# Kernel tuning notes

Measured on AMD Instinct MI355X. Metric: run time of the kernel, lower is better.

The kernel has to match this reference:

```python
import jax, jax.numpy as jnp
from jax import lax
import numpy as np

V = 30000   # vocab_size
E = 64      # embedding_dim
H = 64      # lstm_units
K = 9       # num_tags
B = 512
T = 512


def setup_inputs() -> dict:
    key = jax.random.key(0)
    ks = jax.random.split(key, 12)
    s = 0.05
    return {
        "tokens": jax.random.randint(ks[0], (B, T), 0, V),
        "emb":   jax.random.normal(ks[1], (V + 1, E), dtype=jnp.float32) * s,
        "Wf": jax.random.normal(ks[2], (E, 4 * H), dtype=jnp.float32) * s,
        "Uf": jax.random.normal(ks[3], (H, 4 * H), dtype=jnp.float32) * s,
        "bf": jnp.zeros((4 * H,), dtype=jnp.float32),
        "Wb": jax.random.normal(ks[4], (E, 4 * H), dtype=jnp.float32) * s,
        "Ub": jax.random.normal(ks[5], (H, 4 * H), dtype=jnp.float32) * s,
        "bb": jnp.zeros((4 * H,), dtype=jnp.float32),
        "Wd": jax.random.normal(ks[6], (2 * H, K), dtype=jnp.float32) * s,
        "bd": jnp.zeros((K,), dtype=jnp.float32),
        "trans": jax.random.normal(ks[7], (K, K), dtype=jnp.float32) * s,
    }


def _lstm(x_tm, mask_tm, W, U, b):
    """Keras-convention LSTM over time-major x_tm [T,B,E]; masked steps carry state."""
    Bsz = x_tm.shape[1]
    h0 = jnp.zeros((Bsz, U.shape[0]), x_tm.dtype)
    c0 = jnp.zeros_like(h0)

    def step(carry, inp):
        h, c = carry
        xt, mt = inp                      # xt [B,E], mt [B] bool
        z = xt @ W + h @ U + b            # [B,4H], gate order i,f,g,o
        i, f, g, o = jnp.split(z, 4, axis=-1)
        c_new = jax.nn.sigmoid(f) * c + jax.nn.sigmoid(i) * jnp.tanh(g)
        h_new = jax.nn.sigmoid(o) * jnp.tanh(c_new)
        m = mt[:, None]
        h2 = jnp.where(m, h_new, h)
        c2 = jnp.where(m, c_new, c)
        return (h2, c2), h2

    _, hs = lax.scan(step, (h0, c0), (x_tm, mask_tm))
    return hs                              # [T,B,H]


def _viterbi(pot, mask, trans):
    """Batched Viterbi decode. pot [B,T,K], mask [B,T] bool, trans [K,K]."""
    pot_t = pot.transpose(1, 0, 2)         # [T,B,K]
    m_t = mask.T                           # [T,B]
    alpha0 = pot_t[0]
    ident = jnp.arange(K, dtype=jnp.int32)[None, :]

    def step(alpha, inp):
        p, m = inp                         # p [B,K], m [B]
        scores = alpha[:, :, None] + trans[None]   # [B, prev K, next K]
        best = scores.max(axis=1)
        bp = scores.argmax(axis=1).astype(jnp.int32)
        mm = m[:, None]
        alpha_new = jnp.where(mm, best + p, alpha)
        bp = jnp.where(mm, bp, ident)
        return alpha_new, bp

    alpha, bps = lax.scan(step, alpha0, (pot_t[1:], m_t[1:]))   # bps [T-1,B,K]
    last = alpha.argmax(axis=-1).astype(jnp.int32)              # [B]

    def back(tag, bp):
        prev = jnp.take_along_axis(bp, tag[:, None], axis=1)[:, 0]
        return prev, prev

    _, ys = lax.scan(back, last, bps, reverse=True)             # ys[t] = tag_t, t<T-1
    tags = jnp.concatenate([ys, last[None]], axis=0).T          # [B,T]
    return jnp.where(mask, tags, 0)


def reference(tokens, emb, Wf, Uf, bf, Wb, Ub, bb, Wd, bd, trans):
    mask = tokens != 0                     # mask_zero semantics
    x = emb[tokens]                        # [B,T,E]
    x_tm = x.transpose(1, 0, 2)            # [T,B,E]
    m_tm = mask.T
    hf = _lstm(x_tm, m_tm, Wf, Uf, bf)                     # forward dir
    hb = _lstm(x_tm[::-1], m_tm[::-1], Wb, Ub, bb)[::-1]   # backward dir
    h = jnp.concatenate([hf, hb], axis=-1).transpose(1, 0, 2)  # [B,T,2H]
    potentials = h @ Wd + bd               # CRF emission potentials [B,T,K]
    decoded = _viterbi(potentials, mask, trans)
    seq_len = mask.sum(axis=1).astype(jnp.int32)
    return decoded, potentials, seq_len
```

## Files before the change

kernel.cpp:

```cpp
#include <hip/hip_runtime.h>

#define BB 512
#define TT 512
#define KK 9
#define VP1 30001
#define BTK ((size_t)BB * TT * KK)

typedef __attribute__((ext_vector_type(8))) short short8;
typedef __attribute__((ext_vector_type(4))) float float4v;

__device__ __forceinline__ float sigm(float x) {
    return __builtin_amdgcn_rcpf(1.0f + __expf(-x));
}
__device__ __forceinline__ float tanh_(float x) {
    return 1.0f - 2.0f * __builtin_amdgcn_rcpf(__expf(2.0f * x) + 1.0f);
}

__device__ __forceinline__ unsigned short f2bf(float f) {
    unsigned int u = __float_as_uint(f);
    unsigned int r = u + 0x7fffu + ((u >> 16) & 1u);
    return (unsigned short)(r >> 16);
}
__device__ __forceinline__ float bflo2f(unsigned int d) { return __uint_as_float(d << 16); }
__device__ __forceinline__ float bfhi2f(unsigned int d) { return __uint_as_float(d & 0xffff0000u); }

__device__ __forceinline__ float bcast(float v, int i) {
    return __uint_as_float(__builtin_amdgcn_readlane(__float_as_uint(v), i));
}

__device__ __forceinline__ void block_sync_lds() {
    __builtin_amdgcn_s_waitcnt(0xC07F);
    __builtin_amdgcn_s_barrier();
}

__global__ __launch_bounds__(256)
void wswz_kernel(const float* __restrict__ Wf, const float* __restrict__ bfv,
                 const float* __restrict__ Wb, const float* __restrict__ bbv,
                 unsigned short* __restrict__ wswz, float* __restrict__ bsw)
{
    const int tid = threadIdx.x;
#pragma unroll
    for (int it = 0; it < 16; ++it) {
        int o = blockIdx.x * 4096 + it * 256 + tid;
        int k = o & 63, c = o >> 6;
        int dir = c >> 8, rem = c & 255;
        int u = rem >> 2, g = rem & 3;
        float val = (dir ? Wb : Wf)[k * 256 + g * 64 + u];
        wswz[o] = f2bf(val);
    }
    if (blockIdx.x == 0) {
#pragma unroll
        for (int h = 0; h < 2; ++h) {
            int c = h * 256 + tid;
            int dir = c >> 8, rem = c & 255;
            bsw[c] = (dir ? bbv : bfv)[(rem & 3) * 64 + (rem >> 2)];
        }
    }
}

__global__ __launch_bounds__(256, 1)
void embw_kernel(const float* __restrict__ emb,
                 const unsigned short* __restrict__ wswz, const float* __restrict__ bsw,
                 unsigned short* __restrict__ embw)
{
    const int v0 = blockIdx.x * 64;
    const int tid = threadIdx.x;
    const int w = tid >> 6, lane = tid & 63;
    const int l16 = lane & 15, quad = lane >> 4;

    __shared__ __align__(16) unsigned short clds[64][520];

    short8 bFr[8][2];
    float biasn[8];
#pragma unroll
    for (int n = 0; n < 8; ++n) {
        int c = w * 128 + n * 16 + l16;
        biasn[n] = bsw[c];
        const unsigned short* wp = wswz + c * 64;
#pragma unroll
        for (int q = 0; q < 2; ++q)
            bFr[n][q] = *(const short8*)(wp + q * 32 + quad * 8);
    }

    short8 aFr[4][2];
#pragma unroll
    for (int mt = 0; mt < 4; ++mt) {
        int vrow = v0 + mt * 16 + l16;
        if (vrow >= VP1) vrow = VP1 - 1;
        const float* er = emb + (size_t)vrow * 64;
#pragma unroll
        for (int q = 0; q < 2; ++q) {
            const float* p = er + q * 32 + quad * 8;
            float4 x0 = *(const float4*)(p);
            float4 x1 = *(const float4*)(p + 4);
            short8 v;
            v[0] = (short)f2bf(x0.x); v[1] = (short)f2bf(x0.y);
            v[2] = (short)f2bf(x0.z); v[3] = (short)f2bf(x0.w);
            v[4] = (short)f2bf(x1.x); v[5] = (short)f2bf(x1.y);
            v[6] = (short)f2bf(x1.z); v[7] = (short)f2bf(x1.w);
            aFr[mt][q] = v;
        }
    }

    float4v acc[4][8];
#pragma unroll
    for (int mt = 0; mt < 4; ++mt)
#pragma unroll
        for (int n = 0; n < 8; ++n) {
            acc[mt][n][0] = biasn[n]; acc[mt][n][1] = biasn[n];
            acc[mt][n][2] = biasn[n]; acc[mt][n][3] = biasn[n];
        }
#pragma unroll
    for (int mt = 0; mt < 4; ++mt)
#pragma unroll
        for (int n = 0; n < 8; ++n) {
            acc[mt][n] = __builtin_amdgcn_mfma_f32_16x16x32_bf16(aFr[mt][0], bFr[n][0], acc[mt][n], 0, 0, 0);
            acc[mt][n] = __builtin_amdgcn_mfma_f32_16x16x32_bf16(aFr[mt][1], bFr[n][1], acc[mt][n], 0, 0, 0);
        }

#pragma unroll
    for (int mt = 0; mt < 4; ++mt)
#pragma unroll
        for (int n = 0; n < 8; ++n) {
            int cc = w * 128 + n * 16 + l16;
#pragma unroll
            for (int r = 0; r < 4; ++r)
                clds[mt * 16 + quad * 4 + r][cc] = f2bf(acc[mt][n][r]);
        }
    __syncthreads();

#pragma unroll
    for (int it = 0; it < 16; ++it) {
        int idx = it * 256 + tid;
        int row = idx >> 6, chunk = idx & 63;
        if (v0 + row < VP1) {
            uint4 val = *(const uint4*)&clds[row][chunk * 8];
            *(uint4*)(embw + (size_t)(v0 + row) * 512 + chunk * 8) = val;
        }
    }
}

__global__ __launch_bounds__(256, 1)
void rec_kernel(const int* __restrict__ tokens,
                const unsigned short* __restrict__ embw,
                const float* __restrict__ Uf, const float* __restrict__ Ub,
                const float* __restrict__ Wd,
                float* __restrict__ potf, float* __restrict__ potb)
{
    const int blk = blockIdx.x;
    const int dir = blk >> 7;
    const int row0 = (blk & 127) * 4;
    const int tid = threadIdx.x;
    const int lane = tid & 63;
    const int w = tid >> 6;
    const int l16 = lane & 15, quad = lane >> 4;
    const int u = w * 16 + l16;

    const float* Up = dir ? Ub : Uf;
    float* pot = dir ? potb : potf;
    const uint2* ebase = (const uint2*)embw + dir * 64 + u;

    __shared__ int tokl[4][TT];
    __shared__ __align__(16) unsigned short hl[2][16][72];

    for (int i = tid; i < 2 * 16 * 72; i += 256)
        ((unsigned short*)hl)[i] = 0;
    for (int i = tid; i < 4 * TT; i += 256) {
        int r = i >> 9, t = i & 511;
        tokl[r][t] = tokens[(row0 + r) * TT + t];
    }

    short8 bU[4][2];
#pragma unroll
    for (int g = 0; g < 4; ++g)
#pragma unroll
        for (int q = 0; q < 2; ++q) {
            short8 v;
#pragma unroll
            for (int j = 0; j < 8; ++j) {
                int k = q * 32 + quad * 8 + j;
                v[j] = (short)f2bf(Up[k * 256 + g * 64 + u]);
            }
            bU[g][q] = v;
        }
    short8 bW[2];
#pragma unroll
    for (int q = 0; q < 2; ++q) {
        short8 v;
#pragma unroll
        for (int j = 0; j < 8; ++j) {
            int k = q * 32 + quad * 8 + j;
            v[j] = (l16 < KK) ? (short)f2bf(Wd[(dir * 64 + k) * KK + l16]) : (short)0;
        }
        bW[q] = v;
    }

    __syncthreads();

    int tokA[4], tokB[4];
    uint2 zxp[4];
#pragma unroll
    for (int d = 0; d < 4; ++d) {
        int td = dir ? (TT - 1 - d) : d;
        int td4 = dir ? (TT - 1 - (d + 4)) : (d + 4);
        tokA[d] = tokl[quad][td];
        tokB[d] = tokl[quad][td4];
    }
#pragma unroll
    for (int d = 0; d < 4; ++d)
        zxp[d] = ebase[(size_t)tokA[d] << 7];

    float c_st = 0.f, h_st = 0.f;

    float4v accg[4];
#pragma unroll
    for (int g = 0; g < 4; ++g) {
        accg[g][0] = 0.f; accg[g][1] = 0.f; accg[g][2] = 0.f; accg[g][3] = 0.f;
    }

    const int tprev0 = dir ? (w == 0 ? TT - 4 : TT - w) : (w == 0 ? 3 : w - 1);
    int vOff = (((row0 + quad) * TT + tprev0) * KK + l16) * 4;
    const int vStep = (dir ? -4 : 4) * KK * 4;

    for (int sb = 0; sb < TT; sb += 4) {
#pragma unroll
        for (int ss = 0; ss < 4; ++ss) {
            const int s = sb + ss;
            int tcur = tokA[ss];
            uint2 zcur = zxp[ss];

            hl[ss & 1][quad * 4][u] = f2bf(h_st);

            if (s + 4 < TT)
                zxp[ss] = ebase[(size_t)tokB[ss] << 7];
            tokA[ss] = tokB[ss];

            block_sync_lds();

            const unsigned short* hrow = &hl[ss & 1][l16][0];
            short8 a0 = *(const short8*)(hrow + quad * 8);
            short8 a1 = *(const short8*)(hrow + 32 + quad * 8);

            if (s + 8 < TT) {
                int t8 = dir ? (TT - 1 - (s + 8)) : (s + 8);
                tokB[ss] = tokl[quad][t8];
            }

            accg[0][0] = bflo2f(zcur.x);
            accg[1][0] = bfhi2f(zcur.x);
            accg[2][0] = bflo2f(zcur.y);
            accg[3][0] = bfhi2f(zcur.y);
#pragma unroll
            for (int g = 0; g < 4; ++g) {
                accg[g] = __builtin_amdgcn_mfma_f32_16x16x32_bf16(a0, bU[g][0], accg[g], 0, 0, 0);
                accg[g] = __builtin_amdgcn_mfma_f32_16x16x32_bf16(a1, bU[g][1], accg[g], 0, 0, 0);
            }

            if (w == ss && s > 0) {
                float4v accP = {0.f, 0.f, 0.f, 0.f};
                accP = __builtin_amdgcn_mfma_f32_16x16x32_bf16(a0, bW[0], accP, 0, 0, 0);
                accP = __builtin_amdgcn_mfma_f32_16x16x32_bf16(a1, bW[1], accP, 0, 0, 0);
                if (l16 < KK)
                    *(float*)((char*)pot + vOff) = accP[0];
                vOff += vStep;
            }

            {
                float zi = accg[0][0], zf = accg[1][0], zg = accg[2][0], zo = accg[3][0];
                float cn = sigm(zf) * c_st + sigm(zi) * tanh_(zg);
                float hn = sigm(zo) * tanh_(cn);
                bool m = (tcur != 0);
                h_st = m ? hn : h_st;
                c_st = m ? cn : c_st;
            }
        }
    }

    hl[0][quad * 4][u] = f2bf(h_st);
    block_sync_lds();
    if (w == 0) {
        const unsigned short* hrow = &hl[0][l16][0];
        short8 a0 = *(const short8*)(hrow + quad * 8);
        short8 a1 = *(const short8*)(hrow + 32 + quad * 8);
        float4v accP = {0.f, 0.f, 0.f, 0.f};
        accP = __builtin_amdgcn_mfma_f32_16x16x32_bf16(a0, bW[0], accP, 0, 0, 0);
        accP = __builtin_amdgcn_mfma_f32_16x16x32_bf16(a1, bW[1], accP, 0, 0, 0);
        int tlast = dir ? 0 : (TT - 1);
        if (l16 < KK)
            pot[((size_t)(row0 + quad) * TT + tlast) * KK + l16] = accP[0];
    }
}

__global__ __launch_bounds__(64)
void viterbi_kernel(const int* __restrict__ tokens,
                    const float* __restrict__ potf, const float* __restrict__ potb,
                    const float* __restrict__ bd, const float* __restrict__ trans,
                    float* __restrict__ dec_out, float* __restrict__ pot_out,
                    float* __restrict__ seq_out)
{
    const int row = blockIdx.x;
    const int lane = threadIdx.x;

    __shared__ float pl[TT * KK + 16];
    __shared__ unsigned char bpl[(TT - 1) * KK];
    __shared__ unsigned char maskl[TT + 8];
    __shared__ unsigned char segmap[64][KK];
    __shared__ unsigned char bseq[65];
    __shared__ float decl_[TT];
    __shared__ float bdl[16];

    if (lane < KK) bdl[lane] = bd[lane];
    if (lane < 8) maskl[TT + lane] = 0;
    pl[TT * KK + lane % 16] = 0.f;

    int cnt = 0;
#pragma unroll
    for (int ch = 0; ch < TT / 64; ++ch) {
        int tk = tokens[row * TT + ch * 64 + lane];
        int m = (tk != 0) ? 1 : 0;
        maskl[ch * 64 + lane] = (unsigned char)m;
        cnt += m;
    }
    for (int off = 32; off > 0; off >>= 1) cnt += __shfl_down(cnt, off);
    if (lane == 0) seq_out[row] = (float)cnt;

    const size_t base = (size_t)row * (TT * KK);
    int r9 = lane % KK;
    for (int i = 0; i < (TT * KK) / 64; ++i) {
        int li = i * 64 + lane;
        float s = potf[base + li] + potb[base + li] + bdl[r9];
        pl[li] = s;
        pot_out[base + li] = s;
        r9 = (r9 + 1 == KK) ? 0 : r9 + 1;
    }
    __syncthreads();

    float treg[KK];
#pragma unroll
    for (int i = 0; i < KK; ++i) treg[i] = (lane < KK) ? trans[i * KK + lane] : 0.f;

    float alpha = (lane < KK) ? pl[lane] : -1e30f;
    float pnext = (lane < KK) ? pl[KK + lane] : 0.f;
    int mnext = maskl[1];
#pragma unroll 4
    for (int t = 1; t < TT; ++t) {
        float p = pnext;
        int m = mnext;
        pnext = (lane < KK) ? pl[(t + 1) * KK + lane] : 0.f;
        mnext = maskl[t + 1];

        float sc[KK];
#pragma unroll
        for (int i = 0; i < KK; ++i) sc[i] = bcast(alpha, i) + treg[i];
        float b0 = fmaxf(fmaxf(fmaxf(sc[0], sc[1]), sc[2]),
                   fmaxf(fmaxf(fmaxf(sc[3], sc[4]), sc[5]),
                         fmaxf(fmaxf(sc[6], sc[7]), sc[8])));
        int i0 = 8;
#pragma unroll
        for (int i = 7; i >= 0; --i) i0 = (sc[i] == b0) ? i : i0;

        alpha = m ? (b0 + p) : alpha;
        int bpv = m ? i0 : lane;
        if (lane < KK) bpl[(t - 1) * KK + lane] = (unsigned char)bpv;
    }
    float sc[KK];
#pragma unroll
    for (int i = 0; i < KK; ++i) sc[i] = bcast(alpha, i);
    float b0 = fmaxf(fmaxf(fmaxf(sc[0], sc[1]), sc[2]),
               fmaxf(fmaxf(fmaxf(sc[3], sc[4]), sc[5]),
                     fmaxf(fmaxf(sc[6], sc[7]), sc[8])));
    int last = 8;
#pragma unroll
    for (int i = 7; i >= 0; --i) last = (sc[i] == b0) ? i : last;
    __syncthreads();

    {
        int l = lane;
#pragma unroll
        for (int x = 0; x < KK; ++x) {
            int y = x;
#pragma unroll
            for (int d = 7; d >= 0; --d) {
                int t = 8 * l + d;
                if (t < TT - 1) y = bpl[t * KK + y];
            }
            segmap[l][x] = (unsigned char)y;
        }
    }
    __syncthreads();
    if (lane == 0) {
        int cur = last;
        bseq[64] = (unsigned char)last;
        for (int l = 63; l >= 0; --l) {
            cur = segmap[l][cur];
            bseq[l] = (unsigned char)cur;
        }
    }
    __syncthreads();
    {
        int l = lane;
        int cur = bseq[l + 1];
#pragma unroll
        for (int d = 7; d >= 0; --d) {
            int t = 8 * l + d;
            if (t < TT - 1) cur = bpl[t * KK + cur];
            decl_[t] = (maskl[t] != 0) ? (float)cur : 0.f;
        }
    }
    __syncthreads();
#pragma unroll
    for (int ch = 0; ch < TT / 64; ++ch)
        dec_out[(size_t)row * TT + ch * 64 + lane] = decl_[ch * 64 + lane];
}

extern "C" void kernel_launch(void* const* d_in, const int* in_sizes, int n_in,
                              void* d_out, int out_size, void* d_ws, size_t ws_size,
                              hipStream_t stream)
{
    const int*   tokens = (const int*)d_in[0];
    const float* emb    = (const float*)d_in[1];
    const float* Wf     = (const float*)d_in[2];
    const float* Uf     = (const float*)d_in[3];
    const float* bfv    = (const float*)d_in[4];
    const float* Wb     = (const float*)d_in[5];
    const float* Ub     = (const float*)d_in[6];
    const float* bbv    = (const float*)d_in[7];
    const float* Wd     = (const float*)d_in[8];
    const float* bd     = (const float*)d_in[9];
    const float* trans  = (const float*)d_in[10];

    float* out     = (float*)d_out;
    float* dec_out = out;
    float* pot_out = out + (size_t)BB * TT;
    float* seq_out = out + (size_t)BB * TT + BTK;

    float* potf = (float*)d_ws;
    float* potb = potf + BTK;
    unsigned short* embw = (unsigned short*)(potb + BTK);
    unsigned short* wswz = (unsigned short*)potf;
    float* bsw = (float*)((char*)potf + 512 * 64 * sizeof(unsigned short));

    hipLaunchKernelGGL(wswz_kernel, dim3(8), dim3(256), 0, stream,
                       Wf, bfv, Wb, bbv, wswz, bsw);
    hipLaunchKernelGGL(embw_kernel, dim3(469), dim3(256), 0, stream,
                       emb, wswz, bsw, embw);
    hipLaunchKernelGGL(rec_kernel, dim3(256), dim3(256), 0, stream,
                       tokens, embw, Uf, Ub, Wd, potf, potb);
    hipLaunchKernelGGL(viterbi_kernel, dim3(BB), dim3(64), 0, stream,
                       tokens, potf, potb, bd, trans, dec_out, pot_out, seq_out);
}
```

Before: 401.1 us.

## Run each LSTM recurrence in a single wavefront with bpermute h exchange

The recurrence kernel moves from four wavefronts per block, which shared h through LDS with a block barrier every timestep, to a single 64-lane wavefront that computes all 16 gate column tiles itself. The hidden state is redistributed into the MFMA A-operand layout with ds_bpermute, and the precomputed input projections are re-swizzled to match. This removes per-step barriers and LDS round trips from the serial critical path. In exchange each wave issues four times as many MFMAs per step, holds more registers, and the grid drops to 256 single-wave blocks, so latency per step could rise.

Measured after the change: 727.4 us. +81.3%, slower.

```diff
diff --git a/kernel.cpp b/kernel.cpp
--- a/kernel.cpp
+++ b/kernel.cpp
@@ -8,6 +8,7 @@
 
 typedef __attribute__((ext_vector_type(8))) short short8;
 typedef __attribute__((ext_vector_type(4))) float float4v;
+typedef __attribute__((ext_vector_type(4))) int int4v;
 
 __device__ __forceinline__ float sigm(float x) {
     return __builtin_amdgcn_rcpf(1.0f + __expf(-x));
@@ -26,11 +27,6 @@
 
 __device__ __forceinline__ float bcast(float v, int i) {
     return __uint_as_float(__builtin_amdgcn_readlane(__float_as_uint(v), i));
-}
-
-__device__ __forceinline__ void block_sync_lds() {
-    __builtin_amdgcn_s_waitcnt(0xC07F);
-    __builtin_amdgcn_s_barrier();
 }
 
 __global__ __launch_bounds__(256)
@@ -44,7 +40,9 @@
         int o = blockIdx.x * 4096 + it * 256 + tid;
         int k = o & 63, c = o >> 6;
         int dir = c >> 8, rem = c & 255;
-        int u = rem >> 2, g = rem & 3;
+        int l16p = rem >> 4, idx = rem & 15;
+        int un = idx >> 2, g = idx & 3;
+        int u = un * 16 + l16p;
         float val = (dir ? Wb : Wf)[k * 256 + g * 64 + u];
         wswz[o] = f2bf(val);
     }
@@ -53,7 +51,9 @@
         for (int h = 0; h < 2; ++h) {
             int c = h * 256 + tid;
             int dir = c >> 8, rem = c & 255;
-            bsw[c] = (dir ? bbv : bfv)[(rem & 3) * 64 + (rem >> 2)];
+            int l16p = rem >> 4, idx = rem & 15;
+            int un = idx >> 2, g = idx & 3;
+            bsw[c] = (dir ? bbv : bfv)[g * 64 + un * 16 + l16p];
         }
     }
 }
@@ -140,7 +140,7 @@
     }
 }
 
-__global__ __launch_bounds__(256, 1)
+__global__ __launch_bounds__(64, 1)
 void rec_kernel(const int* __restrict__ tokens,
                 const unsigned short* __restrict__ embw,
                 const float* __restrict__ Uf, const float* __restrict__ Ub,
@@ -149,39 +149,33 @@
 {
     const int blk = blockIdx.x;
     const int dir = blk >> 7;
-    const int row0 = (blk & 127) * 4;
-    const int tid = threadIdx.x;
-    const int lane = tid & 63;
-    const int w = tid >> 6;
+    const int r0 = (blk & 127) * 4;
+    const int lane = threadIdx.x;
     const int l16 = lane & 15, quad = lane >> 4;
-    const int u = w * 16 + l16;
 
     const float* Up = dir ? Ub : Uf;
     float* pot = dir ? potb : potf;
-    const uint2* ebase = (const uint2*)embw + dir * 64 + u;
-
-    __shared__ int tokl[4][TT];
-    __shared__ __align__(16) unsigned short hl[2][16][72];
-
-    for (int i = tid; i < 2 * 16 * 72; i += 256)
-        ((unsigned short*)hl)[i] = 0;
-    for (int i = tid; i < 4 * TT; i += 256) {
-        int r = i >> 9, t = i & 511;
-        tokl[r][t] = tokens[(row0 + r) * TT + t];
-    }
-
-    short8 bU[4][2];
-#pragma unroll
-    for (int g = 0; g < 4; ++g)
+
+    __shared__ int tokl[4][520];
+
+    for (int i = lane; i < 4 * TT; i += 64) {
+        int r = i >> 9, s = i & 511;
+        tokl[r][s] = tokens[(r0 + r) * TT + (dir ? (TT - 1 - s) : s)];
+    }
+
+    short8 bU[16][2];
+#pragma unroll
+    for (int nt = 0; nt < 16; ++nt)
 #pragma unroll
         for (int q = 0; q < 2; ++q) {
             short8 v;
 #pragma unroll
             for (int j = 0; j < 8; ++j) {
                 int k = q * 32 + quad * 8 + j;
-                v[j] = (short)f2bf(Up[k * 256 + g * 64 + u]);
-            }
-            bU[g][q] = v;
+                int sk = 16 * (k & 3) + (k >> 2);
+                v[j] = (short)f2bf(Up[sk * 256 + nt * 16 + l16]);
+            }
+            bU[nt][q] = v;
         }
     short8 bW[2];
 #pragma unroll
@@ -190,104 +184,124 @@
 #pragma unroll
         for (int j = 0; j < 8; ++j) {
             int k = q * 32 + quad * 8 + j;
-            v[j] = (l16 < KK) ? (short)f2bf(Wd[(dir * 64 + k) * KK + l16]) : (short)0;
+            int sk = 16 * (k & 3) + (k >> 2);
+            v[j] = (l16 < KK) ? (short)f2bf(Wd[(dir * 64 + sk) * KK + l16]) : (short)0;
         }
         bW[q] = v;
     }
 
-    __syncthreads();
+    const int cb = (l16 >> 2) * 16;
+    const int idxA0 = (cb + quad * 2) * 4;
+    const int idxA1 = (cb + 8 + quad * 2) * 4;
 
     int tokA[4], tokB[4];
-    uint2 zxp[4];
+#pragma unroll
+    for (int d = 0; d < 4; ++d) tokA[d] = tokl[quad][d];
+#pragma unroll
+    for (int d = 0; d < 4; ++d) tokB[d] = tokl[quad][d + 4];
+
+    uint4 zxp[4][2];
 #pragma unroll
     for (int d = 0; d < 4; ++d) {
-        int td = dir ? (TT - 1 - d) : d;
-        int td4 = dir ? (TT - 1 - (d + 4)) : (d + 4);
-        tokA[d] = tokl[quad][td];
-        tokB[d] = tokl[quad][td4];
-    }
-#pragma unroll
-    for (int d = 0; d < 4; ++d)
-        zxp[d] = ebase[(size_t)tokA[d] << 7];
-
-    float c_st = 0.f, h_st = 0.f;
-
-    float4v accg[4];
-#pragma unroll
-    for (int g = 0; g < 4; ++g) {
-        accg[g][0] = 0.f; accg[g][1] = 0.f; accg[g][2] = 0.f; accg[g][3] = 0.f;
-    }
-
-    const int tprev0 = dir ? (w == 0 ? TT - 4 : TT - w) : (w == 0 ? 3 : w - 1);
-    int vOff = (((row0 + quad) * TT + tprev0) * KK + l16) * 4;
-    const int vStep = (dir ? -4 : 4) * KK * 4;
+        const uint4* p = (const uint4*)(embw + (size_t)tokA[d] * 512 + dir * 256 + l16 * 16);
+        zxp[d][0] = p[0]; zxp[d][1] = p[1];
+    }
+
+    float c_st[4] = {0.f, 0.f, 0.f, 0.f};
+    float h_st[4] = {0.f, 0.f, 0.f, 0.f};
+    unsigned int hp0 = 0u, hp1 = 0u;
+
+    float4v acc[16];
+#pragma unroll
+    for (int nt = 0; nt < 16; ++nt) {
+        acc[nt][0] = 0.f; acc[nt][1] = 0.f; acc[nt][2] = 0.f; acc[nt][3] = 0.f;
+    }
+    float4v accP = {0.f, 0.f, 0.f, 0.f};
+
+    int vOff = ((r0 + quad) * TT + (dir ? (TT - 1) : 0)) * KK + l16;
+    const int vStep = dir ? -KK : KK;
+    const bool potAct = (l16 < KK);
 
     for (int sb = 0; sb < TT; sb += 4) {
 #pragma unroll
         for (int ss = 0; ss < 4; ++ss) {
             const int s = sb + ss;
-            int tcur = tokA[ss];
-            uint2 zcur = zxp[ss];
-
-            hl[ss & 1][quad * 4][u] = f2bf(h_st);
-
-            if (s + 4 < TT)
-                zxp[ss] = ebase[(size_t)tokB[ss] << 7];
+            const int tcur = tokA[ss];
+            const uint4 z0 = zxp[ss][0], z1 = zxp[ss][1];
+
+            if (s + 4 < TT) {
+                const uint4* p = (const uint4*)(embw + (size_t)tokB[ss] * 512 + dir * 256 + l16 * 16);
+                zxp[ss][0] = p[0]; zxp[ss][1] = p[1];
+            }
             tokA[ss] = tokB[ss];
-
-            block_sync_lds();
-
-            const unsigned short* hrow = &hl[ss & 1][l16][0];
-            short8 a0 = *(const short8*)(hrow + quad * 8);
-            short8 a1 = *(const short8*)(hrow + 32 + quad * 8);
-
-            if (s + 8 < TT) {
-                int t8 = dir ? (TT - 1 - (s + 8)) : (s + 8);
-                tokB[ss] = tokl[quad][t8];
-            }
-
-            accg[0][0] = bflo2f(zcur.x);
-            accg[1][0] = bfhi2f(zcur.x);
-            accg[2][0] = bflo2f(zcur.y);
-            accg[3][0] = bfhi2f(zcur.y);
-#pragma unroll
-            for (int g = 0; g < 4; ++g) {
-                accg[g] = __builtin_amdgcn_mfma_f32_16x16x32_bf16(a0, bU[g][0], accg[g], 0, 0, 0);
-                accg[g] = __builtin_amdgcn_mfma_f32_16x16x32_bf16(a1, bU[g][1], accg[g], 0, 0, 0);
-            }
-
-            if (w == ss && s > 0) {
-                float4v accP = {0.f, 0.f, 0.f, 0.f};
+            if (s + 8 < TT) tokB[ss] = tokl[quad][s + 8];
+
+            int4v ai0, ai1;
+            ai0.x = __builtin_amdgcn_ds_bpermute(idxA0,     (int)hp0);
+            ai0.y = __builtin_amdgcn_ds_bpermute(idxA0,     (int)hp1);
+            ai0.z = __builtin_amdgcn_ds_bpermute(idxA0 + 4, (int)hp0);
+            ai0.w = __builtin_amdgcn_ds_bpermute(idxA0 + 4, (int)hp1);
+            ai1.x = __builtin_amdgcn_ds_bpermute(idxA1,     (int)hp0);
+            ai1.y = __builtin_amdgcn_ds_bpermute(idxA1,     (int)hp1);
+            ai1.z = __builtin_amdgcn_ds_bpermute(idxA1 + 4, (int)hp0);
+            ai1.w = __builtin_amdgcn_ds_bpermute(idxA1 + 4, (int)hp1);
+            short8 a0 = __builtin_bit_cast(short8, ai0);
+            short8 a1 = __builtin_bit_cast(short8, ai1);
+
+            acc[0][0]  = bflo2f(z0.x);  acc[4][0]  = bfhi2f(z0.x);
+            acc[8][0]  = bflo2f(z0.y);  acc[12][0] = bfhi2f(z0.y);
+            acc[1][0]  = bflo2f(z0.z);  acc[5][0]  = bfhi2f(z0.z);
+            acc[9][0]  = bflo2f(z0.w);  acc[13][0] = bfhi2f(z0.w);
+            acc[2][0]  = bflo2f(z1.x);  acc[6][0]  = bfhi2f(z1.x);
+            acc[10][0] = bflo2f(z1.y);  acc[14][0] = bfhi2f(z1.y);
+            acc[3][0]  = bflo2f(z1.z);  acc[7][0]  = bfhi2f(z1.z);
+            acc[11][0] = bflo2f(z1.w);  acc[15][0] = bfhi2f(z1.w);
+
+#pragma unroll
+            for (int nt = 0; nt < 16; ++nt) {
+                acc[nt] = __builtin_amdgcn_mfma_f32_16x16x32_bf16(a0, bU[nt][0], acc[nt], 0, 0, 0);
+                acc[nt] = __builtin_amdgcn_mfma_f32_16x16x32_bf16(a1, bU[nt][1], acc[nt], 0, 0, 0);
+            }
+
+            if (s > 0) {
+                accP[0] = 0.f;
                 accP = __builtin_amdgcn_mfma_f32_16x16x32_bf16(a0, bW[0], accP, 0, 0, 0);
                 accP = __builtin_amdgcn_mfma_f32_16x16x32_bf16(a1, bW[1], accP, 0, 0, 0);
-                if (l16 < KK)
-                    *(float*)((char*)pot + vOff) = accP[0];
+                if (potAct) pot[vOff] = accP[0];
                 vOff += vStep;
             }
 
-            {
-                float zi = accg[0][0], zf = accg[1][0], zg = accg[2][0], zo = accg[3][0];
-                float cn = sigm(zf) * c_st + sigm(zi) * tanh_(zg);
+            const bool m = (tcur != 0);
+#pragma unroll
+            for (int un = 0; un < 4; ++un) {
+                float zi = acc[un][0], zf = acc[4 + un][0];
+                float zg = acc[8 + un][0], zo = acc[12 + un][0];
+                float cn = sigm(zf) * c_st[un] + sigm(zi) * tanh_(zg);
                 float hn = sigm(zo) * tanh_(cn);
-                bool m = (tcur != 0);
-                h_st = m ? hn : h_st;
-                c_st = m ? cn : c_st;
-            }
-        }
-    }
-
-    hl[0][quad * 4][u] = f2bf(h_st);
-    block_sync_lds();
-    if (w == 0) {
-        const unsigned short* hrow = &hl[0][l16][0];
-        short8 a0 = *(const short8*)(hrow + quad * 8);
-        short8 a1 = *(const short8*)(hrow + 32 + quad * 8);
-        float4v accP = {0.f, 0.f, 0.f, 0.f};
+                h_st[un] = m ? hn : h_st[un];
+                c_st[un] = m ? cn : c_st[un];
+            }
+            hp0 = (unsigned)f2bf(h_st[0]) | ((unsigned)f2bf(h_st[1]) << 16);
+            hp1 = (unsigned)f2bf(h_st[2]) | ((unsigned)f2bf(h_st[3]) << 16);
+        }
+    }
+
+    {
+        int4v ai0, ai1;
+        ai0.x = __builtin_amdgcn_ds_bpermute(idxA0,     (int)hp0);
+        ai0.y = __builtin_amdgcn_ds_bpermute(idxA0,     (int)hp1);
+        ai0.z = __builtin_amdgcn_ds_bpermute(idxA0 + 4, (int)hp0);
+        ai0.w = __builtin_amdgcn_ds_bpermute(idxA0 + 4, (int)hp1);
+        ai1.x = __builtin_amdgcn_ds_bpermute(idxA1,     (int)hp0);
+        ai1.y = __builtin_amdgcn_ds_bpermute(idxA1,     (int)hp1);
+        ai1.z = __builtin_amdgcn_ds_bpermute(idxA1 + 4, (int)hp0);
+        ai1.w = __builtin_amdgcn_ds_bpermute(idxA1 + 4, (int)hp1);
+        short8 a0 = __builtin_bit_cast(short8, ai0);
+        short8 a1 = __builtin_bit_cast(short8, ai1);
+        accP[0] = 0.f;
         accP = __builtin_amdgcn_mfma_f32_16x16x32_bf16(a0, bW[0], accP, 0, 0, 0);
         accP = __builtin_amdgcn_mfma_f32_16x16x32_bf16(a1, bW[1], accP, 0, 0, 0);
-        int tlast = dir ? 0 : (TT - 1);
-        if (l16 < KK)
-            pot[((size_t)(row0 + quad) * TT + tlast) * KK + l16] = accP[0];
+        if (potAct) pot[vOff] = accP[0];
     }
 }
 
@@ -444,7 +458,7 @@
                        Wf, bfv, Wb, bbv, wswz, bsw);
     hipLaunchKernelGGL(embw_kernel, dim3(469), dim3(256), 0, stream,
                        emb, wswz, bsw, embw);
-    hipLaunchKernelGGL(rec_kernel, dim3(256), dim3(256), 0, stream,
+    hipLaunchKernelGGL(rec_kernel, dim3(256), dim3(64), 0, stream,
                        tokens, embw, Uf, Ub, Wd, potf, potb);
     hipLaunchKernelGGL(viterbi_kernel, dim3(BB), dim3(64), 0, stream,
                        tokens, potf, potb, bd, trans, dec_out, pot_out, seq_out);
```

## Halve recurrence block to two waves, each thread owning two hidden units

Applied to the files above, without the earlier changes.

The LSTM recurrence kernel drops from four waves to two per block. Each lane now computes two hidden units, so it issues twice as many MFMAs and does two cell updates per step. The precomputed input-projection table is re-swizzled so one 16-byte load fetches both units' gate pre-activations, and the tokens are stored pre-reversed for the backward direction. The aim is a cheaper per-step block barrier and fewer waves synchronising on the serial critical path, at the cost of more serial work per wave on each step.

Measured after the change: 496.8 us. 23.9% more time.

```diff
diff --git a/kernel.cpp b/kernel.cpp
--- a/kernel.cpp
+++ b/kernel.cpp
@@ -44,8 +44,9 @@
         int o = blockIdx.x * 4096 + it * 256 + tid;
         int k = o & 63, c = o >> 6;
         int dir = c >> 8, rem = c & 255;
-        int u = rem >> 2, g = rem & 3;
-        float val = (dir ? Wb : Wf)[k * 256 + g * 64 + u];
+        int wv = rem >> 7, l16 = (rem >> 3) & 15, hh = (rem >> 2) & 1, g = rem & 3;
+        int gatecol = g * 64 + wv * 32 + l16 * 2 + hh;
+        float val = (dir ? Wb : Wf)[k * 256 + gatecol];
         wswz[o] = f2bf(val);
     }
     if (blockIdx.x == 0) {
@@ -53,7 +54,9 @@
         for (int h = 0; h < 2; ++h) {
             int c = h * 256 + tid;
             int dir = c >> 8, rem = c & 255;
-            bsw[c] = (dir ? bbv : bfv)[(rem & 3) * 64 + (rem >> 2)];
+            int wv = rem >> 7, l16 = (rem >> 3) & 15, hh = (rem >> 2) & 1, g = rem & 3;
+            int gatecol = g * 64 + wv * 32 + l16 * 2 + hh;
+            bsw[c] = (dir ? bbv : bfv)[gatecol];
         }
     }
 }
@@ -140,7 +143,7 @@
     }
 }
 
-__global__ __launch_bounds__(256, 1)
+__global__ __launch_bounds__(128, 1)
 void rec_kernel(const int* __restrict__ tokens,
                 const unsigned short* __restrict__ embw,
                 const float* __restrict__ Uf, const float* __restrict__ Ub,
@@ -149,40 +152,40 @@
 {
     const int blk = blockIdx.x;
     const int dir = blk >> 7;
-    const int row0 = (blk & 127) * 4;
+    const int r0 = (blk & 127) * 4;
     const int tid = threadIdx.x;
+    const int wv = tid >> 6;
     const int lane = tid & 63;
-    const int w = tid >> 6;
     const int l16 = lane & 15, quad = lane >> 4;
-    const int u = w * 16 + l16;
 
     const float* Up = dir ? Ub : Uf;
     float* pot = dir ? potb : potf;
-    const uint2* ebase = (const uint2*)embw + dir * 64 + u;
-
-    __shared__ int tokl[4][TT];
+
+    __shared__ int tokl[4][TT + 8];
     __shared__ __align__(16) unsigned short hl[2][16][72];
 
-    for (int i = tid; i < 2 * 16 * 72; i += 256)
+    for (int i = tid; i < 2 * 16 * 72; i += 128)
         ((unsigned short*)hl)[i] = 0;
-    for (int i = tid; i < 4 * TT; i += 256) {
-        int r = i >> 9, t = i & 511;
-        tokl[r][t] = tokens[(row0 + r) * TT + t];
-    }
-
-    short8 bU[4][2];
+    for (int i = tid; i < 4 * TT; i += 128) {
+        int r = i >> 9, s = i & 511;
+        tokl[r][s] = tokens[(r0 + r) * TT + (dir ? (TT - 1 - s) : s)];
+    }
+
+    short8 bU[4][2][2];
 #pragma unroll
     for (int g = 0; g < 4; ++g)
 #pragma unroll
-        for (int q = 0; q < 2; ++q) {
-            short8 v;
-#pragma unroll
-            for (int j = 0; j < 8; ++j) {
-                int k = q * 32 + quad * 8 + j;
-                v[j] = (short)f2bf(Up[k * 256 + g * 64 + u]);
+        for (int hh = 0; hh < 2; ++hh)
+#pragma unroll
+            for (int q = 0; q < 2; ++q) {
+                short8 v;
+#pragma unroll
+                for (int j = 0; j < 8; ++j) {
+                    int k = q * 32 + quad * 8 + j;
+                    v[j] = (short)f2bf(Up[k * 256 + g * 64 + wv * 32 + l16 * 2 + hh]);
+                }
+                bU[g][hh][q] = v;
             }
-            bU[g][q] = v;
-        }
     short8 bW[2];
 #pragma unroll
     for (int q = 0; q < 2; ++q) {
@@ -198,41 +201,43 @@
     __syncthreads();
 
     int tokA[4], tokB[4];
-    uint2 zxp[4];
-#pragma unroll
-    for (int d = 0; d < 4; ++d) {
-        int td = dir ? (TT - 1 - d) : d;
-        int td4 = dir ? (TT - 1 - (d + 4)) : (d + 4);
-        tokA[d] = tokl[quad][td];
-        tokB[d] = tokl[quad][td4];
-    }
+#pragma unroll
+    for (int d = 0; d < 4; ++d) { tokA[d] = tokl[quad][d]; tokB[d] = tokl[quad][d + 4]; }
+
+    const unsigned short* ebase = embw + dir * 256 + wv * 128 + l16 * 8;
+    uint4 zxp[4];
 #pragma unroll
     for (int d = 0; d < 4; ++d)
-        zxp[d] = ebase[(size_t)tokA[d] << 7];
-
-    float c_st = 0.f, h_st = 0.f;
-
-    float4v accg[4];
-#pragma unroll
-    for (int g = 0; g < 4; ++g) {
-        accg[g][0] = 0.f; accg[g][1] = 0.f; accg[g][2] = 0.f; accg[g][3] = 0.f;
-    }
-
-    const int tprev0 = dir ? (w == 0 ? TT - 4 : TT - w) : (w == 0 ? 3 : w - 1);
-    int vOff = (((row0 + quad) * TT + tprev0) * KK + l16) * 4;
-    const int vStep = (dir ? -4 : 4) * KK * 4;
+        zxp[d] = *(const uint4*)(ebase + (size_t)tokA[d] * 512);
+
+    float c0 = 0.f, c1 = 0.f, h0 = 0.f, h1 = 0.f;
+
+    float4v acc[4][2];
+#pragma unroll
+    for (int g = 0; g < 4; ++g)
+#pragma unroll
+        for (int hh = 0; hh < 2; ++hh) {
+            acc[g][hh][0] = 0.f; acc[g][hh][1] = 0.f;
+            acc[g][hh][2] = 0.f; acc[g][hh][3] = 0.f;
+        }
+
+    const int myT0 = (wv == 1) ? 0 : 1;
+    int vOff = ((r0 + quad) * TT + (dir ? (TT - 1 - myT0) : myT0)) * KK + l16;
+    const int vStep = (dir ? -2 : 2) * KK;
+    const bool potAct = (l16 < KK);
 
     for (int sb = 0; sb < TT; sb += 4) {
 #pragma unroll
         for (int ss = 0; ss < 4; ++ss) {
             const int s = sb + ss;
-            int tcur = tokA[ss];
-            uint2 zcur = zxp[ss];
-
-            hl[ss & 1][quad * 4][u] = f2bf(h_st);
+            const int tcur = tokA[ss];
+            const uint4 z = zxp[ss];
+
+            *(unsigned int*)&hl[ss & 1][quad * 4][wv * 32 + l16 * 2] =
+                (unsigned int)f2bf(h0) | ((unsigned int)f2bf(h1) << 16);
 
             if (s + 4 < TT)
-                zxp[ss] = ebase[(size_t)tokB[ss] << 7];
+                zxp[ss] = *(const uint4*)(ebase + (size_t)tokB[ss] * 512);
             tokA[ss] = tokB[ss];
 
             block_sync_lds();
@@ -241,44 +246,51 @@
             short8 a0 = *(const short8*)(hrow + quad * 8);
             short8 a1 = *(const short8*)(hrow + 32 + quad * 8);
 
-            if (s + 8 < TT) {
-                int t8 = dir ? (TT - 1 - (s + 8)) : (s + 8);
-                tokB[ss] = tokl[quad][t8];
-            }
-
-            accg[0][0] = bflo2f(zcur.x);
-            accg[1][0] = bfhi2f(zcur.x);
-            accg[2][0] = bflo2f(zcur.y);
-            accg[3][0] = bfhi2f(zcur.y);
-#pragma unroll
-            for (int g = 0; g < 4; ++g) {
-                accg[g] = __builtin_amdgcn_mfma_f32_16x16x32_bf16(a0, bU[g][0], accg[g], 0, 0, 0);
-                accg[g] = __builtin_amdgcn_mfma_f32_16x16x32_bf16(a1, bU[g][1], accg[g], 0, 0, 0);
-            }
-
-            if (w == ss && s > 0) {
+            if (s + 8 < TT) tokB[ss] = tokl[quad][s + 8];
+
+            acc[0][0][0] = bflo2f(z.x); acc[1][0][0] = bfhi2f(z.x);
+            acc[2][0][0] = bflo2f(z.y); acc[3][0][0] = bfhi2f(z.y);
+            acc[0][1][0] = bflo2f(z.z); acc[1][1][0] = bfhi2f(z.z);
+            acc[2][1][0] = bflo2f(z.w); acc[3][1][0] = bfhi2f(z.w);
+
+#pragma unroll
+            for (int g = 0; g < 4; ++g)
+#pragma unroll
+                for (int hh = 0; hh < 2; ++hh) {
+                    acc[g][hh] = __builtin_amdgcn_mfma_f32_16x16x32_bf16(a0, bU[g][hh][0], acc[g][hh], 0, 0, 0);
+                    acc[g][hh] = __builtin_amdgcn_mfma_f32_16x16x32_bf16(a1, bU[g][hh][1], acc[g][hh], 0, 0, 0);
+                }
+
+            if (wv == (ss & 1) && s > 0) {
                 float4v accP = {0.f, 0.f, 0.f, 0.f};
                 accP = __builtin_amdgcn_mfma_f32_16x16x32_bf16(a0, bW[0], accP, 0, 0, 0);
                 accP = __builtin_amdgcn_mfma_f32_16x16x32_bf16(a1, bW[1], accP, 0, 0, 0);
-                if (l16 < KK)
-                    *(float*)((char*)pot + vOff) = accP[0];
+                if (potAct) pot[vOff] = accP[0];
                 vOff += vStep;
             }
 
+            const bool m = (tcur != 0);
             {
-                float zi = accg[0][0], zf = accg[1][0], zg = accg[2][0], zo = accg[3][0];
-                float cn = sigm(zf) * c_st + sigm(zi) * tanh_(zg);
+                float zi = acc[0][0][0], zf = acc[1][0][0];
+                float zg = acc[2][0][0], zo = acc[3][0][0];
+                float cn = sigm(zf) * c0 + sigm(zi) * tanh_(zg);
                 float hn = sigm(zo) * tanh_(cn);
-                bool m = (tcur != 0);
-                h_st = m ? hn : h_st;
-                c_st = m ? cn : c_st;
+                h0 = m ? hn : h0; c0 = m ? cn : c0;
             }
-        }
-    }
-
-    hl[0][quad * 4][u] = f2bf(h_st);
+            {
+                float zi = acc[0][1][0], zf = acc[1][1][0];
+                float zg = acc[2][1][0], zo = acc[3][1][0];
+                float cn = sigm(zf) * c1 + sigm(zi) * tanh_(zg);
+                float hn = sigm(zo) * tanh_(cn);
+                h1 = m ? hn : h1; c1 = m ? cn : c1;
+            }
+        }
+    }
+
+    *(unsigned int*)&hl[0][quad * 4][wv * 32 + l16 * 2] =
+        (unsigned int)f2bf(h0) | ((unsigned int)f2bf(h1) << 16);
     block_sync_lds();
-    if (w == 0) {
+    if (wv == 0) {
         const unsigned short* hrow = &hl[0][l16][0];
         short8 a0 = *(const short8*)(hrow + quad * 8);
         short8 a1 = *(const short8*)(hrow + 32 + quad * 8);
@@ -286,8 +298,8 @@
         accP = __builtin_amdgcn_mfma_f32_16x16x32_bf16(a0, bW[0], accP, 0, 0, 0);
         accP = __builtin_amdgcn_mfma_f32_16x16x32_bf16(a1, bW[1], accP, 0, 0, 0);
         int tlast = dir ? 0 : (TT - 1);
-        if (l16 < KK)
-            pot[((size_t)(row0 + quad) * TT + tlast) * KK + l16] = accP[0];
+        if (potAct)
+            pot[((size_t)(r0 + quad) * TT + tlast) * KK + l16] = accP[0];
     }
 }
 
@@ -444,7 +456,7 @@
                        Wf, bfv, Wb, bbv, wswz, bsw);
     hipLaunchKernelGGL(embw_kernel, dim3(469), dim3(256), 0, stream,
                        emb, wswz, bsw, embw);
-    hipLaunchKernelGGL(rec_kernel, dim3(256), dim3(256), 0, stream,
+    hipLaunchKernelGGL(rec_kernel, dim3(256), dim3(128), 0, stream,
                        tokens, embw, Uf, Ub, Wd, potf, potb);
     hipLaunchKernelGGL(viterbi_kernel, dim3(BB), dim3(64), 0, stream,
                        tokens, potf, potb, bd, trans, dec_out, pot_out, seq_out);
```

## Offload emission projection to a dedicated wave and split recurrent MFMA chains

Applied to the files above, without the earlier changes.

The recurrent kernel gains a fifth wave that computes the per-step emission projection (h·Wd) and writes the potentials. This takes that work off the four gate waves, which previously took turns doing it inside the serial time loop. The gate MFMAs are split into two independent accumulator chains that are summed afterwards, to shorten the dependent MFMA latency on the critical path, and the activation order is rearranged. The Viterbi kernel moves to 128 threads so the potential summation and output copies use two waves, while the serial decode stays on one wave. The extra wave joins every per-step barrier, which may add synchronisation cost.

Measured after the change: 372.2 us. -7.2%, faster.

```diff
diff --git a/kernel.cpp b/kernel.cpp
--- a/kernel.cpp
+++ b/kernel.cpp
@@ -140,7 +140,7 @@
     }
 }
 
-__global__ __launch_bounds__(256, 1)
+__global__ __launch_bounds__(320, 1)
 void rec_kernel(const int* __restrict__ tokens,
                 const unsigned short* __restrict__ embw,
                 const float* __restrict__ Uf, const float* __restrict__ Ub,
@@ -151,147 +151,156 @@
     const int dir = blk >> 7;
     const int row0 = (blk & 127) * 4;
     const int tid = threadIdx.x;
+    const int wv = tid >> 6;
     const int lane = tid & 63;
-    const int w = tid >> 6;
     const int l16 = lane & 15, quad = lane >> 4;
-    const int u = w * 16 + l16;
 
     const float* Up = dir ? Ub : Uf;
     float* pot = dir ? potb : potf;
-    const uint2* ebase = (const uint2*)embw + dir * 64 + u;
-
-    __shared__ int tokl[4][TT];
+
+    __shared__ int tokl[4][TT + 8];
     __shared__ __align__(16) unsigned short hl[2][16][72];
 
-    for (int i = tid; i < 2 * 16 * 72; i += 256)
+    for (int i = tid; i < 2 * 16 * 72; i += 320)
         ((unsigned short*)hl)[i] = 0;
-    for (int i = tid; i < 4 * TT; i += 256) {
+    for (int i = tid; i < 4 * TT; i += 320) {
         int r = i >> 9, t = i & 511;
         tokl[r][t] = tokens[(row0 + r) * TT + t];
     }
 
-    short8 bU[4][2];
-#pragma unroll
-    for (int g = 0; g < 4; ++g)
+    if (wv < 4) {
+        const int w = wv;
+        const int u = w * 16 + l16;
+
+        short8 bU[4][2];
+#pragma unroll
+        for (int g = 0; g < 4; ++g)
+#pragma unroll
+            for (int q = 0; q < 2; ++q) {
+                short8 v;
+#pragma unroll
+                for (int j = 0; j < 8; ++j) {
+                    int k = q * 32 + quad * 8 + j;
+                    v[j] = (short)f2bf(Up[k * 256 + g * 64 + u]);
+                }
+                bU[g][q] = v;
+            }
+
+        __syncthreads();
+
+        int tokA[4], tokB[4];
+        const uint2* ebase = (const uint2*)embw + dir * 64 + u;
+#pragma unroll
+        for (int d = 0; d < 4; ++d) {
+            int td = dir ? (TT - 1 - d) : d;
+            int td4 = dir ? (TT - 1 - (d + 4)) : (d + 4);
+            tokA[d] = tokl[quad][td];
+            tokB[d] = tokl[quad][td4];
+        }
+        uint2 zxp[4];
+#pragma unroll
+        for (int d = 0; d < 4; ++d)
+            zxp[d] = ebase[(size_t)tokA[d] << 7];
+
+        float c_st = 0.f, h_st = 0.f;
+        float4v accA[4], accB[4];
+        const float4v zz = {0.f, 0.f, 0.f, 0.f};
+#pragma unroll
+        for (int g = 0; g < 4; ++g) { accA[g] = zz; accB[g] = zz; }
+
+        for (int sb = 0; sb < TT; sb += 4) {
+#pragma unroll
+            for (int ss = 0; ss < 4; ++ss) {
+                const int s = sb + ss;
+                const int tcur = tokA[ss];
+                const uint2 zcur = zxp[ss];
+
+                hl[ss & 1][quad * 4][u] = f2bf(h_st);
+
+                if (s + 4 < TT)
+                    zxp[ss] = ebase[(size_t)tokB[ss] << 7];
+                tokA[ss] = tokB[ss];
+
+                block_sync_lds();
+
+                const unsigned short* hrow = &hl[ss & 1][l16][0];
+                short8 a0 = *(const short8*)(hrow + quad * 8);
+                short8 a1 = *(const short8*)(hrow + 32 + quad * 8);
+
+                if (s + 8 < TT) {
+                    int t8 = dir ? (TT - 1 - (s + 8)) : (s + 8);
+                    tokB[ss] = tokl[quad][t8];
+                }
+
+                accA[0][0] = bflo2f(zcur.x);
+                accA[1][0] = bfhi2f(zcur.x);
+                accA[2][0] = bflo2f(zcur.y);
+                accA[3][0] = bfhi2f(zcur.y);
+
+                accA[2] = __builtin_amdgcn_mfma_f32_16x16x32_bf16(a0, bU[2][0], accA[2], 0, 0, 0);
+                accB[2] = __builtin_amdgcn_mfma_f32_16x16x32_bf16(a1, bU[2][1], zz, 0, 0, 0);
+                accA[0] = __builtin_amdgcn_mfma_f32_16x16x32_bf16(a0, bU[0][0], accA[0], 0, 0, 0);
+                accB[0] = __builtin_amdgcn_mfma_f32_16x16x32_bf16(a1, bU[0][1], zz, 0, 0, 0);
+                accA[1] = __builtin_amdgcn_mfma_f32_16x16x32_bf16(a0, bU[1][0], accA[1], 0, 0, 0);
+                accB[1] = __builtin_amdgcn_mfma_f32_16x16x32_bf16(a1, bU[1][1], zz, 0, 0, 0);
+                accA[3] = __builtin_amdgcn_mfma_f32_16x16x32_bf16(a0, bU[3][0], accA[3], 0, 0, 0);
+                accB[3] = __builtin_amdgcn_mfma_f32_16x16x32_bf16(a1, bU[3][1], zz, 0, 0, 0);
+
+                {
+                    float zg_ = accA[2][0] + accB[2][0];
+                    float tg  = tanh_(zg_);
+                    float zi_ = accA[0][0] + accB[0][0];
+                    float si  = sigm(zi_);
+                    float zf_ = accA[1][0] + accB[1][0];
+                    float zo_ = accA[3][0] + accB[3][0];
+                    float cn  = sigm(zf_) * c_st + si * tg;
+                    float hn  = sigm(zo_) * tanh_(cn);
+                    bool m = (tcur != 0);
+                    h_st = m ? hn : h_st;
+                    c_st = m ? cn : c_st;
+                }
+            }
+        }
+
+        hl[0][quad * 4][u] = f2bf(h_st);
+        block_sync_lds();
+    } else {
+        short8 bW[2];
 #pragma unroll
         for (int q = 0; q < 2; ++q) {
             short8 v;
 #pragma unroll
             for (int j = 0; j < 8; ++j) {
                 int k = q * 32 + quad * 8 + j;
-                v[j] = (short)f2bf(Up[k * 256 + g * 64 + u]);
+                v[j] = (l16 < KK) ? (short)f2bf(Wd[(dir * 64 + k) * KK + l16]) : (short)0;
             }
-            bU[g][q] = v;
-        }
-    short8 bW[2];
-#pragma unroll
-    for (int q = 0; q < 2; ++q) {
-        short8 v;
-#pragma unroll
-        for (int j = 0; j < 8; ++j) {
-            int k = q * 32 + quad * 8 + j;
-            v[j] = (l16 < KK) ? (short)f2bf(Wd[(dir * 64 + k) * KK + l16]) : (short)0;
-        }
-        bW[q] = v;
-    }
-
-    __syncthreads();
-
-    int tokA[4], tokB[4];
-    uint2 zxp[4];
-#pragma unroll
-    for (int d = 0; d < 4; ++d) {
-        int td = dir ? (TT - 1 - d) : d;
-        int td4 = dir ? (TT - 1 - (d + 4)) : (d + 4);
-        tokA[d] = tokl[quad][td];
-        tokB[d] = tokl[quad][td4];
-    }
-#pragma unroll
-    for (int d = 0; d < 4; ++d)
-        zxp[d] = ebase[(size_t)tokA[d] << 7];
-
-    float c_st = 0.f, h_st = 0.f;
-
-    float4v accg[4];
-#pragma unroll
-    for (int g = 0; g < 4; ++g) {
-        accg[g][0] = 0.f; accg[g][1] = 0.f; accg[g][2] = 0.f; accg[g][3] = 0.f;
-    }
-
-    const int tprev0 = dir ? (w == 0 ? TT - 4 : TT - w) : (w == 0 ? 3 : w - 1);
-    int vOff = (((row0 + quad) * TT + tprev0) * KK + l16) * 4;
-    const int vStep = (dir ? -4 : 4) * KK * 4;
-
-    for (int sb = 0; sb < TT; sb += 4) {
-#pragma unroll
-        for (int ss = 0; ss < 4; ++ss) {
-            const int s = sb + ss;
-            int tcur = tokA[ss];
-            uint2 zcur = zxp[ss];
-
-            hl[ss & 1][quad * 4][u] = f2bf(h_st);
-
-            if (s + 4 < TT)
-                zxp[ss] = ebase[(size_t)tokB[ss] << 7];
-            tokA[ss] = tokB[ss];
-
+            bW[q] = v;
+        }
+
+        __syncthreads();
+
+        int vOff = ((row0 + quad) * TT + (dir ? (TT - 1) : 0)) * KK + l16;
+        const int vStep = dir ? -KK : KK;
+        const bool potAct = (l16 < KK);
+        const float4v zz = {0.f, 0.f, 0.f, 0.f};
+
+        for (int s = 0; s <= TT; ++s) {
             block_sync_lds();
-
-            const unsigned short* hrow = &hl[ss & 1][l16][0];
+            const unsigned short* hrow = &hl[s & 1][l16][0];
             short8 a0 = *(const short8*)(hrow + quad * 8);
             short8 a1 = *(const short8*)(hrow + 32 + quad * 8);
-
-            if (s + 8 < TT) {
-                int t8 = dir ? (TT - 1 - (s + 8)) : (s + 8);
-                tokB[ss] = tokl[quad][t8];
-            }
-
-            accg[0][0] = bflo2f(zcur.x);
-            accg[1][0] = bfhi2f(zcur.x);
-            accg[2][0] = bflo2f(zcur.y);
-            accg[3][0] = bfhi2f(zcur.y);
-#pragma unroll
-            for (int g = 0; g < 4; ++g) {
-                accg[g] = __builtin_amdgcn_mfma_f32_16x16x32_bf16(a0, bU[g][0], accg[g], 0, 0, 0);
-                accg[g] = __builtin_amdgcn_mfma_f32_16x16x32_bf16(a1, bU[g][1], accg[g], 0, 0, 0);
-            }
-
-            if (w == ss && s > 0) {
-                float4v accP = {0.f, 0.f, 0.f, 0.f};
-                accP = __builtin_amdgcn_mfma_f32_16x16x32_bf16(a0, bW[0], accP, 0, 0, 0);
+            if (s > 0) {
+                float4v accP;
+                accP = __builtin_amdgcn_mfma_f32_16x16x32_bf16(a0, bW[0], zz, 0, 0, 0);
                 accP = __builtin_amdgcn_mfma_f32_16x16x32_bf16(a1, bW[1], accP, 0, 0, 0);
-                if (l16 < KK)
-                    *(float*)((char*)pot + vOff) = accP[0];
+                if (potAct) pot[vOff] = accP[0];
                 vOff += vStep;
             }
-
-            {
-                float zi = accg[0][0], zf = accg[1][0], zg = accg[2][0], zo = accg[3][0];
-                float cn = sigm(zf) * c_st + sigm(zi) * tanh_(zg);
-                float hn = sigm(zo) * tanh_(cn);
-                bool m = (tcur != 0);
-                h_st = m ? hn : h_st;
-                c_st = m ? cn : c_st;
-            }
-        }
-    }
-
-    hl[0][quad * 4][u] = f2bf(h_st);
-    block_sync_lds();
-    if (w == 0) {
-        const unsigned short* hrow = &hl[0][l16][0];
-        short8 a0 = *(const short8*)(hrow + quad * 8);
-        short8 a1 = *(const short8*)(hrow + 32 + quad * 8);
-        float4v accP = {0.f, 0.f, 0.f, 0.f};
-        accP = __builtin_amdgcn_mfma_f32_16x16x32_bf16(a0, bW[0], accP, 0, 0, 0);
-        accP = __builtin_amdgcn_mfma_f32_16x16x32_bf16(a1, bW[1], accP, 0, 0, 0);
-        int tlast = dir ? 0 : (TT - 1);
-        if (l16 < KK)
-            pot[((size_t)(row0 + quad) * TT + tlast) * KK + l16] = accP[0];
-    }
-}
-
-__global__ __launch_bounds__(64)
+        }
+    }
+}
+
+__global__ __launch_bounds__(128)
 void viterbi_kernel(const int* __restrict__ tokens,
                     const float* __restrict__ potf, const float* __restrict__ potb,
                     const float* __restrict__ bd, const float* __restrict__ trans,
@@ -299,7 +308,9 @@
                     float* __restrict__ seq_out)
 {
     const int row = blockIdx.x;
-    const int lane = threadIdx.x;
+    const int L = threadIdx.x;
+    const int wave = L >> 6;
+    const int lane = L & 63;
 
     __shared__ float pl[TT * KK + 16];
     __shared__ unsigned char bpl[(TT - 1) * KK];
@@ -309,72 +320,80 @@
     __shared__ float decl_[TT];
     __shared__ float bdl[16];
 
-    if (lane < KK) bdl[lane] = bd[lane];
-    if (lane < 8) maskl[TT + lane] = 0;
-    pl[TT * KK + lane % 16] = 0.f;
-
-    int cnt = 0;
-#pragma unroll
-    for (int ch = 0; ch < TT / 64; ++ch) {
-        int tk = tokens[row * TT + ch * 64 + lane];
-        int m = (tk != 0) ? 1 : 0;
-        maskl[ch * 64 + lane] = (unsigned char)m;
-        cnt += m;
-    }
-    for (int off = 32; off > 0; off >>= 1) cnt += __shfl_down(cnt, off);
-    if (lane == 0) seq_out[row] = (float)cnt;
+    if (L < KK) bdl[L] = bd[L];
+    if (L < 8) maskl[TT + L] = 0;
+    pl[TT * KK + (L & 15)] = 0.f;
+
+    if (wave == 0) {
+        int cnt = 0;
+#pragma unroll
+        for (int ch = 0; ch < TT / 64; ++ch) {
+            int tk = tokens[row * TT + ch * 64 + lane];
+            int m = (tk != 0) ? 1 : 0;
+            maskl[ch * 64 + lane] = (unsigned char)m;
+            cnt += m;
+        }
+        for (int off = 32; off > 0; off >>= 1) cnt += __shfl_down(cnt, off);
+        if (lane == 0) seq_out[row] = (float)cnt;
+    }
+    __syncthreads();
 
     const size_t base = (size_t)row * (TT * KK);
-    int r9 = lane % KK;
-    for (int i = 0; i < (TT * KK) / 64; ++i) {
-        int li = i * 64 + lane;
-        float s = potf[base + li] + potb[base + li] + bdl[r9];
-        pl[li] = s;
-        pot_out[base + li] = s;
-        r9 = (r9 + 1 == KK) ? 0 : r9 + 1;
-    }
-    __syncthreads();
-
-    float treg[KK];
-#pragma unroll
-    for (int i = 0; i < KK; ++i) treg[i] = (lane < KK) ? trans[i * KK + lane] : 0.f;
-
-    float alpha = (lane < KK) ? pl[lane] : -1e30f;
-    float pnext = (lane < KK) ? pl[KK + lane] : 0.f;
-    int mnext = maskl[1];
+    {
+        int r9 = L % KK;
+        for (int i = L; i < TT * KK; i += 128) {
+            float s = potf[base + i] + potb[base + i] + bdl[r9];
+            pl[i] = s;
+            pot_out[base + i] = s;
+            r9 += 2;
+            if (r9 >= KK) r9 -= KK;
+        }
+    }
+    __syncthreads();
+
+    int last = 0;
+    if (wave == 0) {
+        float treg[KK];
+#pragma unroll
+        for (int i = 0; i < KK; ++i) treg[i] = (lane < KK) ? trans[i * KK + lane] : 0.f;
+
+        float alpha = (lane < KK) ? pl[lane] : -1e30f;
+        float pnext = (lane < KK) ? pl[KK + lane] : 0.f;
+        int mnext = maskl[1];
 #pragma unroll 4
-    for (int t = 1; t < TT; ++t) {
-        float p = pnext;
-        int m = mnext;
-        pnext = (lane < KK) ? pl[(t + 1) * KK + lane] : 0.f;
-        mnext = maskl[t + 1];
-
+        for (int t = 1; t < TT; ++t) {
+            float p = pnext;
+            int m = mnext;
+            pnext = (lane < KK) ? pl[(t + 1) * KK + lane] : 0.f;
+            mnext = maskl[t + 1];
+
+            float sc[KK];
+#pragma unroll
+            for (int i = 0; i < KK; ++i) sc[i] = bcast(alpha, i) + treg[i];
+            float b0 = fmaxf(fmaxf(fmaxf(sc[0], sc[1]), sc[2]),
+                       fmaxf(fmaxf(fmaxf(sc[3], sc[4]), sc[5]),
+                             fmaxf(fmaxf(sc[6], sc[7]), sc[8])));
+            int i0 = 8;
+#pragma unroll
+            for (int i = 7; i >= 0; --i) i0 = (sc[i] == b0) ? i : i0;
+
+            alpha = m ? (b0 + p) : alpha;
+            int bpv = m ? i0 : lane;
+            if (lane < KK) bpl[(t - 1) * KK + lane] = (unsigned char)bpv;
+        }
         float sc[KK];
 #pragma unroll
-        for (int i = 0; i < KK; ++i) sc[i] = bcast(alpha, i) + treg[i];
+        for (int i = 0; i < KK; ++i) sc[i] = bcast(alpha, i);
         float b0 = fmaxf(fmaxf(fmaxf(sc[0], sc[1]), sc[2]),
                    fmaxf(fmaxf(fmaxf(sc[3], sc[4]), sc[5]),
                          fmaxf(fmaxf(sc[6], sc[7]), sc[8])));
-        int i0 = 8;
-#pragma unroll
-        for (int i = 7; i >= 0; --i) i0 = (sc[i] == b0) ? i : i0;
-
-        alpha = m ? (b0 + p) : alpha;
-        int bpv = m ? i0 : lane;
-        if (lane < KK) bpl[(t - 1) * KK + lane] = (unsigned char)bpv;
-    }
-    float sc[KK];
-#pragma unroll
-    for (int i = 0; i < KK; ++i) sc[i] = bcast(alpha, i);
-    float b0 = fmaxf(fmaxf(fmaxf(sc[0], sc[1]), sc[2]),
-               fmaxf(fmaxf(fmaxf(sc[3], sc[4]), sc[5]),
-                     fmaxf(fmaxf(sc[6], sc[7]), sc[8])));
-    int last = 8;
-#pragma unroll
-    for (int i = 7; i >= 0; --i) last = (sc[i] == b0) ? i : last;
-    __syncthreads();
-
-    {
+        last = 8;
+#pragma unroll
+        for (int i = 7; i >= 0; --i) last = (sc[i] == b0) ? i : last;
+    }
+    __syncthreads();
+
+    if (wave == 0) {
         int l = lane;
 #pragma unroll
         for (int x = 0; x < KK; ++x) {
@@ -388,7 +407,7 @@
         }
     }
     __syncthreads();
-    if (lane == 0) {
+    if (L == 0) {
         int cur = last;
         bseq[64] = (unsigned char)last;
         for (int l = 63; l >= 0; --l) {
@@ -397,7 +416,7 @@
         }
     }
     __syncthreads();
-    {
+    if (wave == 0) {
         int l = lane;
         int cur = bseq[l + 1];
 #pragma unroll
@@ -408,9 +427,8 @@
         }
     }
     __syncthreads();
-#pragma unroll
-    for (int ch = 0; ch < TT / 64; ++ch)
-        dec_out[(size_t)row * TT + ch * 64 + lane] = decl_[ch * 64 + lane];
+    for (int i = L; i < TT; i += 128)
+        dec_out[(size_t)row * TT + i] = decl_[i];
 }
 
 extern "C" void kernel_launch(void* const* d_in, const int* in_sizes, int n_in,
@@ -444,8 +462,8 @@
                        Wf, bfv, Wb, bbv, wswz, bsw);
     hipLaunchKernelGGL(embw_kernel, dim3(469), dim3(256), 0, stream,
                        emb, wswz, bsw, embw);
-    hipLaunchKernelGGL(rec_kernel, dim3(256), dim3(256), 0, stream,
+    hipLaunchKernelGGL(rec_kernel, dim3(256), dim3(320), 0, stream,
                        tokens, embw, Uf, Ub, Wd, potf, potb);
-    hipLaunchKernelGGL(viterbi_kernel, dim3(BB), dim3(64), 0, stream,
+    hipLaunchKernelGGL(viterbi_kernel, dim3(BB), dim3(128), 0, stream,
                        tokens, potf, potb, bd, trans, dec_out, pot_out, seq_out);
 }
```
